# Optimization experiments

Hardware: AMD Instinct MI355X
Metric: run time of the kernel (lower is better)

The kernel has to match this reference:

```python
import jax, jax.numpy as jnp
import numpy as np

D_MODEL = 384
KSIZE = 3
B, L = 32, 512
LN_EPS = 1e-5


def _conv1d_same(x, w, b):
    # x: [B, C_in, L], w: [C_out, C_in, K] -> [B, C_out, L]
    y = jax.lax.conv_general_dilated(
        x, w, window_strides=(1,), padding='SAME',
        dimension_numbers=('NCH', 'OIH', 'NCH'))
    return y + b[None, :, None]


def _conv_fft_block(x, wa, ba, wb, bb):
    # Conv1D_FFT: transpose -> conv/relu -> conv/relu -> transpose back
    h = jnp.transpose(x, (0, 2, 1))            # [B, D, L]
    h = jax.nn.relu(_conv1d_same(h, wa, ba))
    h = jax.nn.relu(_conv1d_same(h, wb, bb))
    return jnp.transpose(h, (0, 2, 1))         # [B, L, D]


def _layernorm(x, g, b):
    mu = jnp.mean(x, axis=-1, keepdims=True)
    var = jnp.var(x, axis=-1, keepdims=True)
    return (x - mu) * jax.lax.rsqrt(var + LN_EPS) * g + b


def setup_inputs() -> dict:
    key = jax.random.key(0)
    ks = jax.random.split(key, 8)
    x = jax.random.normal(ks[0], (B, L, D_MODEL), dtype=jnp.float32)
    durations = jax.random.randint(ks[1], (B, L), 0, 8, dtype=jnp.int32)
    s = 0.02
    params = {
        'c1a_w': jax.random.normal(ks[2], (D_MODEL, D_MODEL, KSIZE), jnp.float32) * s,
        'c1a_b': jnp.zeros((D_MODEL,), jnp.float32),
        'c1b_w': jax.random.normal(ks[3], (D_MODEL, D_MODEL, KSIZE), jnp.float32) * s,
        'c1b_b': jnp.zeros((D_MODEL,), jnp.float32),
        'ln1_g': jnp.ones((D_MODEL,), jnp.float32),
        'ln1_b': jnp.zeros((D_MODEL,), jnp.float32),
        'c2a_w': jax.random.normal(ks[4], (D_MODEL, D_MODEL, KSIZE), jnp.float32) * s,
        'c2a_b': jnp.zeros((D_MODEL,), jnp.float32),
        'c2b_w': jax.random.normal(ks[5], (D_MODEL, D_MODEL, KSIZE), jnp.float32) * s,
        'c2b_b': jnp.zeros((D_MODEL,), jnp.float32),
        'ln2_g': jnp.ones((D_MODEL,), jnp.float32),
        'ln2_b': jnp.zeros((D_MODEL,), jnp.float32),
        'lin_w': jax.random.normal(ks[6], (D_MODEL, 1), jnp.float32) * s,
        'lin_b': jnp.zeros((1,), jnp.float32),
    }
    return {'x': x, 'durations': durations, **params}


def reference(x, durations, c1a_w, c1a_b, c1b_w, c1b_b, ln1_g, ln1_b,
              c2a_w, c2a_b, c2b_w, c2b_b, ln2_g, ln2_b, lin_w, lin_b):
    # --- DurationPredictor (dropout = identity, eval mode) ---
    h = _conv_fft_block(x, c1a_w, c1a_b, c1b_w, c1b_b)
    h = _layernorm(h, ln1_g, ln1_b)
    h = _conv_fft_block(h, c2a_w, c2a_b, c2b_w, c2b_b)
    h = _layernorm(h, ln2_g, ln2_b)
    dur_preds = (h @ lin_w + lin_b)[..., 0]      # [B, L]

    # --- LR: duration-based expansion via one-hot alignment matmul ---
    total = jnp.sum(durations, axis=-1)          # [B]
    T = int(jnp.max(total))                      # concrete (durations are input data)
    cum = jnp.cumsum(durations, axis=-1)         # [B, L]
    t = jnp.arange(T, dtype=cum.dtype)           # [T]
    # frame t belongs to phoneme j s.t. cum[j-1] <= t < cum[j]
    idx = jax.vmap(lambda c: jnp.searchsorted(c, t, side='right'))(cum)  # [B, T]
    mask = (t[None, :] < total[:, None]).astype(x.dtype)                 # [B, T]
    align = jax.nn.one_hot(idx, x.shape[1], dtype=x.dtype) * mask[:, :, None]  # [B, T, L]
    out = jnp.einsum('btl,bld->btd', align, x)   # [B, T, D]
    return (out, dur_preds)
```

## Files before the change

kernel.cpp:

```cpp
#include <hip/hip_runtime.h>

#define B_   32
#define L_   512
#define D_   384
#define M_   (B_*L_)
#define KTOT (D_*3)
#define LDW  392
#define BROWS 82
#define BUFE (BROWS*LDW)
#define RPBLK 1728
#define RPTOT (4*RPBLK)
#define SCAT  8192
#define ZT    (16*B_)

typedef __bf16 bf16x8 __attribute__((ext_vector_type(8)));
typedef float  floatx4 __attribute__((ext_vector_type(4)));

__global__ __launch_bounds__(256) void mega_prep_lr(const float* __restrict__ wa,
                                                    const float* __restrict__ wb,
                                                    const float* __restrict__ wc,
                                                    const float* __restrict__ wd,
                                                    __bf16* __restrict__ oa,
                                                    __bf16* __restrict__ ob,
                                                    __bf16* __restrict__ oc,
                                                    __bf16* __restrict__ od,
                                                    const int* __restrict__ dur,
                                                    const float* __restrict__ x,
                                                    float* __restrict__ out, int T)
{
    __shared__ int scum[512];
    int bx = blockIdx.x;

    if (bx < RPTOT) {
        int wi  = bx / RPBLK;
        int idx = (bx - wi * RPBLK) * 256 + threadIdx.x;
        const float* w; __bf16* o_;
        switch (wi) {
            case 0:  w = wa; o_ = oa; break;
            case 1:  w = wb; o_ = ob; break;
            case 2:  w = wc; o_ = oc; break;
            default: w = wd; o_ = od; break;
        }
        int j  = idx & 7;
        int l  = (idx >> 3) & 63;
        int ct = idx >> 9;
        int c  = ct / 24;
        int t  = ct - c * 24;
        int o  = t * 16 + (l & 15);
        int kflat = c * 32 + (l >> 4) * 8 + j;
        int s  = kflat / D_;
        int i  = kflat - s * D_;
        o_[idx] = (__bf16)w[(o * D_ + i) * 3 + s];
        return;
    }

    if (bx < RPTOT + SCAT) {
        int sx  = bx - RPTOT;
        int pl0 = sx * 2;
        int b   = pl0 >> 9;
        const int* db = dur + b * L_;
        if (threadIdx.x < 64) {
            int lane = threadIdx.x;
            int v[8], s = 0;
#pragma unroll
            for (int i = 0; i < 8; i++) { v[i] = db[lane * 8 + i]; s += v[i]; }
            int ex = s;
#pragma unroll
            for (int off = 1; off < 64; off <<= 1) {
                int n = __shfl_up(ex, off);
                if (lane >= off) ex += n;
            }
            ex -= s;
            int c = ex;
#pragma unroll
            for (int i = 0; i < 8; i++) { c += v[i]; scum[lane * 8 + i] = c; }
        }
        __syncthreads();
        int sub = threadIdx.x >> 7;
        int q   = threadIdx.x & 127;
        int l   = (pl0 & 511) + sub;
        int e = scum[l];
        int s = l ? scum[l - 1] : 0;
        if (e == s || q >= 96) return;
        int pl = b * L_ + l;
        float4 v = *(const float4*)(x + (size_t)pl * D_ + q * 4);
        float* ob_ = out + ((size_t)b * T) * D_ + q * 4;
        for (int t = s; t < e; ++t)
            *(float4*)(ob_ + (size_t)t * D_) = v;
        return;
    }

    int zb = bx - RPTOT - SCAT;
    int bxi = zb & 15;
    int b   = zb >> 4;
    if (threadIdx.x < 64) {
        int lane = threadIdx.x;
        int s = 0;
#pragma unroll
        for (int i = 0; i < 8; i++) s += dur[b * L_ + lane * 8 + i];
#pragma unroll
        for (int off = 1; off < 64; off <<= 1) s += __shfl_xor(s, off);
        if (lane == 0) scum[0] = s;
    }
    __syncthreads();
    int total = scum[0];
    int nfr = T - total;
    if (nfr <= 0) return;
    float* base = out + ((size_t)b * T + total) * D_;
    int n4 = nfr * 96;
    for (int i = bxi * 256 + threadIdx.x; i < n4; i += 4096) {
        int fr = i / 96, q = i - fr * 96;
        *(float4*)(base + (size_t)fr * D_ + q * 4) = make_float4(0.f, 0.f, 0.f, 0.f);
    }
}

__global__ __launch_bounds__(512, 1) void fused_predictor(
    const float* __restrict__ x,
    const __bf16* __restrict__ w1a, const float* __restrict__ b1a,
    const __bf16* __restrict__ w1b, const float* __restrict__ b1b,
    const float* __restrict__ g1,  const float* __restrict__ e1,
    const __bf16* __restrict__ w2a, const float* __restrict__ b2a,
    const __bf16* __restrict__ w2b, const float* __restrict__ b2b,
    const float* __restrict__ g2,  const float* __restrict__ e2,
    const float* __restrict__ lw,  const float* __restrict__ lb,
    float* __restrict__ out_dur)
{
    extern __shared__ char smem_raw[];
    __bf16* bufA = (__bf16*)smem_raw;
    __bf16* bufB = bufA + BUFE;
    float*  red1 = (float*)(bufB + BUFE);
    float*  red2 = red1 + BROWS * 8;
    float*  minv = red2 + BROWS * 8;

    const int m0 = blockIdx.x * 64;
    const int l0 = m0 & 511;
    const int b0 = m0 - l0;

    const int tid  = threadIdx.x;
    const int wave = tid >> 6;
    const int lane = tid & 63;
    const int quad = lane >> 4;
    const int lx   = lane & 15;
    const int ng   = wave & 3;
    const int mg   = wave >> 2;
    const int mtc  = mg ? 2 : 3;
    const int mtb  = mg ? 3 : 0;

    bf16x8 kz;
#pragma unroll
    for (int z = 0; z < 8; z++) kz[z] = (__bf16)0.f;

    for (int c = tid; c < BROWS * 48; c += 512) {
        int beta = c / 48, q = c - beta * 48;
        int l = l0 + beta - 9;
        bf16x8 v = kz;
        if ((unsigned)l < (unsigned)L_) {
            const float* xr = x + (size_t)(b0 + l) * D_ + q * 8;
            const float4 f0 = *(const float4*)xr;
            const float4 f1 = *(const float4*)(xr + 4);
            v[0] = (__bf16)f0.x; v[1] = (__bf16)f0.y; v[2] = (__bf16)f0.z; v[3] = (__bf16)f0.w;
            v[4] = (__bf16)f1.x; v[5] = (__bf16)f1.y; v[6] = (__bf16)f1.z; v[7] = (__bf16)f1.w;
        }
        *(bf16x8*)(&bufA[beta * LDW + q * 8]) = v;
    }
    for (int c = tid; c < 2 * 48; c += 512) {
        int beta = (c < 48) ? 0 : 81, q = c % 48;
        *(bf16x8*)(&bufB[beta * LDW + q * 8]) = kz;
    }
    __syncthreads();

    const int t0   = ng * 6;
    const int col0 = ng * 96 + lx;

    floatx4 acc[3][6];
    bf16x8  bg[3][6];

    for (int st = 0; st < 4; st++) {
        const __bf16* bin  = (st & 1) ? bufB : bufA;
        __bf16*       bout = (st & 1) ? bufA : bufB;
        const __bf16* Wp = (st == 0) ? w1a : (st == 1) ? w1b : (st == 2) ? w2a : w2b;
        const float*  bp = (st == 0) ? b1a : (st == 1) ? b1b : (st == 2) ? b2a : b2b;

#pragma unroll
        for (int mt = 0; mt < 3; mt++)
            if (mt < mtc)
#pragma unroll
                for (int ni = 0; ni < 6; ni++)
#pragma unroll
                    for (int r = 0; r < 4; r++) acc[mt][ni][r] = 0.f;

        const char* pb0 = (const char*)Wp + ((size_t)t0 * 64 + lane) * 16;
        auto loadB = [&](int buf, int n) {
            int it = n / 3, s = n - it * 3;
            const char* p = pb0 + (size_t)(s * 12 + it) * 24576;
#pragma unroll
            for (int ni = 0; ni < 6; ni++)
                bg[buf][ni] = *(const bf16x8*)(p + ni * 1024);
        };
        loadB(0, 0); loadB(1, 1);

        const __bf16* ab = bin + (mtb * 16 + lx) * LDW + quad * 8;
#pragma unroll
        for (int n = 0; n < 36; n++) {
            const int it = n / 3, s = n - it * 3;
            if (n + 2 < 36) loadB((n + 2) % 3, n + 2);
            bf16x8 af[3];
            af[0] = *(const bf16x8*)(ab + (s) * LDW + it * 32);
            af[1] = *(const bf16x8*)(ab + (16 + s) * LDW + it * 32);
            if (mtc == 3)
                af[2] = *(const bf16x8*)(ab + (32 + s) * LDW + it * 32);
            __builtin_amdgcn_s_setprio(1);
#pragma unroll
            for (int ni = 0; ni < 6; ni++) {
                acc[0][ni] = __builtin_amdgcn_mfma_f32_16x16x32_bf16(af[0], bg[n % 3][ni], acc[0][ni], 0, 0, 0);
                acc[1][ni] = __builtin_amdgcn_mfma_f32_16x16x32_bf16(af[1], bg[n % 3][ni], acc[1][ni], 0, 0, 0);
            }
            if (mtc == 3) {
#pragma unroll
                for (int ni = 0; ni < 6; ni++)
                    acc[2][ni] = __builtin_amdgcn_mfma_f32_16x16x32_bf16(af[2], bg[n % 3][ni], acc[2][ni], 0, 0, 0);
            }
            __builtin_amdgcn_s_setprio(0);
        }

        float bv[6];
#pragma unroll
        for (int ni = 0; ni < 6; ni++) bv[ni] = bp[col0 + ni * 16];
#pragma unroll
        for (int mt = 0; mt < 3; mt++)
            if (mt < mtc)
#pragma unroll
                for (int ni = 0; ni < 6; ni++)
#pragma unroll
                    for (int r = 0; r < 4; r++) {
                        float vv = acc[mt][ni][r] + bv[ni];
                        acc[mt][ni][r] = vv > 0.f ? vv : 0.f;
                    }

        if (st == 1 || st == 3) {
#pragma unroll
            for (int mt = 0; mt < 3; mt++)
                if (mt < mtc)
#pragma unroll
                    for (int r = 0; r < 4; r++) {
                        float s1 = 0.f, s2 = 0.f;
#pragma unroll
                        for (int ni = 0; ni < 6; ni++) {
                            s1 += acc[mt][ni][r];
                            s2 += acc[mt][ni][r] * acc[mt][ni][r];
                        }
#pragma unroll
                        for (int d = 1; d < 16; d <<= 1) {
                            s1 += __shfl_xor(s1, d);
                            s2 += __shfl_xor(s2, d);
                        }
                        if (lx == 0) {
                            int beta = (mtb + mt) * 16 + quad * 4 + r + 1;
                            red1[beta * 8 + wave] = s1;
                            red2[beta * 8 + wave] = s2;
                        }
                    }
            __syncthreads();
            if (tid < BROWS) {
                int tile = (tid - 1) >> 4;
                int base = (tile >= 3) ? 4 : 0;
                float s1 = 0.f, s2 = 0.f;
#pragma unroll
                for (int k = 0; k < 4; k++) { s1 += red1[tid * 8 + base + k]; s2 += red2[tid * 8 + base + k]; }
                float mean = s1 * (1.f / D_);
                float var  = s2 * (1.f / D_) - mean * mean;
                minv[tid * 2]     = mean;
                minv[tid * 2 + 1] = rsqrtf(var + 1e-5f);
            }
            __syncthreads();
            const float* gp = (st == 1) ? g1 : g2;
            const float* ep = (st == 1) ? e1 : e2;
            float gv[6], ev[6];
#pragma unroll
            for (int ni = 0; ni < 6; ni++) { gv[ni] = gp[col0 + ni * 16]; ev[ni] = ep[col0 + ni * 16]; }
#pragma unroll
            for (int mt = 0; mt < 3; mt++)
                if (mt < mtc)
#pragma unroll
                    for (int r = 0; r < 4; r++) {
                        int beta = (mtb + mt) * 16 + quad * 4 + r + 1;
                        float mean = minv[beta * 2], inv = minv[beta * 2 + 1];
#pragma unroll
                        for (int ni = 0; ni < 6; ni++)
                            acc[mt][ni][r] = (acc[mt][ni][r] - mean) * inv * gv[ni] + ev[ni];
                    }
            if (st == 1) {
#pragma unroll
                for (int mt = 0; mt < 3; mt++)
                    if (mt < mtc)
#pragma unroll
                        for (int r = 0; r < 4; r++) {
                            int beta = (mtb + mt) * 16 + quad * 4 + r + 1;
                            bool ok = (unsigned)(l0 + beta - 9) < (unsigned)L_;
#pragma unroll
                            for (int ni = 0; ni < 6; ni++)
                                bout[beta * LDW + col0 + ni * 16] = (__bf16)(ok ? acc[mt][ni][r] : 0.f);
                        }
            } else {
                float lwv[6];
#pragma unroll
                for (int ni = 0; ni < 6; ni++) lwv[ni] = lw[col0 + ni * 16];
#pragma unroll
                for (int mt = 0; mt < 3; mt++)
                    if (mt < mtc)
#pragma unroll
                        for (int r = 0; r < 4; r++) {
                            float p = 0.f;
#pragma unroll
                            for (int ni = 0; ni < 6; ni++) p += acc[mt][ni][r] * lwv[ni];
#pragma unroll
                            for (int d = 1; d < 16; d <<= 1) p += __shfl_xor(p, d);
                            if (lx == 0) {
                                int beta = (mtb + mt) * 16 + quad * 4 + r + 1;
                                red1[beta * 8 + wave] = p;
                            }
                        }
                __syncthreads();
                if (tid < 64) {
                    int beta = tid + 9;
                    int tile = (beta - 1) >> 4;
                    int base = (tile >= 3) ? 4 : 0;
                    float sacc = lb[0];
#pragma unroll
                    for (int k = 0; k < 4; k++) sacc += red1[beta * 8 + base + k];
                    out_dur[m0 + tid] = sacc;
                }
            }
        } else {
#pragma unroll
            for (int mt = 0; mt < 3; mt++)
                if (mt < mtc)
#pragma unroll
                    for (int r = 0; r < 4; r++) {
                        int beta = (mtb + mt) * 16 + quad * 4 + r + 1;
                        bool ok = (unsigned)(l0 + beta - 9) < (unsigned)L_;
#pragma unroll
                        for (int ni = 0; ni < 6; ni++)
                            bout[beta * LDW + col0 + ni * 16] = (__bf16)(ok ? acc[mt][ni][r] : 0.f);
                    }
        }
        __syncthreads();
    }
}

extern "C" void kernel_launch(void* const* d_in, const int* in_sizes, int n_in,
                              void* d_out, int out_size, void* d_ws, size_t ws_size,
                              hipStream_t stream) {
    const float* x       = (const float*)d_in[0];
    const int*   dur     = (const int*)d_in[1];
    const float* c1a_w   = (const float*)d_in[2];
    const float* c1a_b   = (const float*)d_in[3];
    const float* c1b_w   = (const float*)d_in[4];
    const float* c1b_b   = (const float*)d_in[5];
    const float* ln1_g   = (const float*)d_in[6];
    const float* ln1_b   = (const float*)d_in[7];
    const float* c2a_w   = (const float*)d_in[8];
    const float* c2a_b   = (const float*)d_in[9];
    const float* c2b_w   = (const float*)d_in[10];
    const float* c2b_b   = (const float*)d_in[11];
    const float* ln2_g   = (const float*)d_in[12];
    const float* ln2_b   = (const float*)d_in[13];
    const float* lin_w   = (const float*)d_in[14];
    const float* lin_b   = (const float*)d_in[15];

    const int T = (out_size - B_ * L_) / (B_ * D_);
    float* out_gather = (float*)d_out;
    float* out_dur    = (float*)d_out + (size_t)B_ * T * D_;

    char* p = (char*)d_ws;
    __bf16* w1a = (__bf16*)p; p += (size_t)D_ * KTOT * 2;
    __bf16* w1b = (__bf16*)p; p += (size_t)D_ * KTOT * 2;
    __bf16* w2a = (__bf16*)p; p += (size_t)D_ * KTOT * 2;
    __bf16* w2b = (__bf16*)p; p += (size_t)D_ * KTOT * 2;

    mega_prep_lr<<<RPTOT + SCAT + ZT, 256, 0, stream>>>(
        c1a_w, c1b_w, c2a_w, c2b_w, w1a, w1b, w2a, w2b,
        dur, x, out_gather, T);

    const size_t smem = (size_t)2 * BUFE * 2 + (BROWS * 8 * 2 + BROWS * 2) * 4;
    static bool attr_set = false;
    if (!attr_set) {
        hipFuncSetAttribute((const void*)fused_predictor,
                            hipFuncAttributeMaxDynamicSharedMemorySize, (int)smem);
        attr_set = true;
    }
    fused_predictor<<<256, 512, smem, stream>>>(
        x, w1a, c1a_b, w1b, c1b_b, ln1_g, ln1_b,
        w2a, c2a_b, w2b, c2b_b, ln2_g, ln2_b,
        lin_w, lin_b, out_dur);
}
```

Before: 228.3 us.

## Merge LR expansion into predictor kernel and single-buffer activations for 2 blocks/CU

Moves the duration-based scatter and zero-fill work out of the weight-repack kernel and into extra blocks of the fused predictor launch, so the memory-bound LR expansion can run alongside the compute-bound conv stack. The ping-pong activation buffers are collapsed into one shared buffer, with an extra barrier before write-back, roughly halving LDS use so launch bounds allow two blocks per CU. This trades extra synchronization per stage and possible register pressure under the tighter occupancy bound for overlap and better latency hiding.

```diff
diff --git a/kernel.cpp b/kernel.cpp
--- a/kernel.cpp
+++ b/kernel.cpp
@@ -10,111 +10,46 @@
 #define BUFE (BROWS*LDW)
 #define RPBLK 1728
 #define RPTOT (4*RPBLK)
-#define SCAT  8192
-#define ZT    (16*B_)
+#define FUSE  256
+#define SCB   4096
+#define ZTB   (8*B_)
+#define SMEM_MEGA (BUFE*2 + (BROWS*8*2 + BROWS*2)*4)
 
 typedef __bf16 bf16x8 __attribute__((ext_vector_type(8)));
 typedef float  floatx4 __attribute__((ext_vector_type(4)));
 
-__global__ __launch_bounds__(256) void mega_prep_lr(const float* __restrict__ wa,
-                                                    const float* __restrict__ wb,
-                                                    const float* __restrict__ wc,
-                                                    const float* __restrict__ wd,
-                                                    __bf16* __restrict__ oa,
-                                                    __bf16* __restrict__ ob,
-                                                    __bf16* __restrict__ oc,
-                                                    __bf16* __restrict__ od,
-                                                    const int* __restrict__ dur,
-                                                    const float* __restrict__ x,
-                                                    float* __restrict__ out, int T)
+__global__ __launch_bounds__(256) void repack_kernel(const float* __restrict__ wa,
+                                                     const float* __restrict__ wb,
+                                                     const float* __restrict__ wc,
+                                                     const float* __restrict__ wd,
+                                                     __bf16* __restrict__ oa,
+                                                     __bf16* __restrict__ ob,
+                                                     __bf16* __restrict__ oc,
+                                                     __bf16* __restrict__ od)
 {
-    __shared__ int scum[512];
     int bx = blockIdx.x;
-
-    if (bx < RPTOT) {
-        int wi  = bx / RPBLK;
-        int idx = (bx - wi * RPBLK) * 256 + threadIdx.x;
-        const float* w; __bf16* o_;
-        switch (wi) {
-            case 0:  w = wa; o_ = oa; break;
-            case 1:  w = wb; o_ = ob; break;
-            case 2:  w = wc; o_ = oc; break;
-            default: w = wd; o_ = od; break;
-        }
-        int j  = idx & 7;
-        int l  = (idx >> 3) & 63;
-        int ct = idx >> 9;
-        int c  = ct / 24;
-        int t  = ct - c * 24;
-        int o  = t * 16 + (l & 15);
-        int kflat = c * 32 + (l >> 4) * 8 + j;
-        int s  = kflat / D_;
-        int i  = kflat - s * D_;
-        o_[idx] = (__bf16)w[(o * D_ + i) * 3 + s];
-        return;
-    }
-
-    if (bx < RPTOT + SCAT) {
-        int sx  = bx - RPTOT;
-        int pl0 = sx * 2;
-        int b   = pl0 >> 9;
-        const int* db = dur + b * L_;
-        if (threadIdx.x < 64) {
-            int lane = threadIdx.x;
-            int v[8], s = 0;
-#pragma unroll
-            for (int i = 0; i < 8; i++) { v[i] = db[lane * 8 + i]; s += v[i]; }
-            int ex = s;
-#pragma unroll
-            for (int off = 1; off < 64; off <<= 1) {
-                int n = __shfl_up(ex, off);
-                if (lane >= off) ex += n;
-            }
-            ex -= s;
-            int c = ex;
-#pragma unroll
-            for (int i = 0; i < 8; i++) { c += v[i]; scum[lane * 8 + i] = c; }
-        }
-        __syncthreads();
-        int sub = threadIdx.x >> 7;
-        int q   = threadIdx.x & 127;
-        int l   = (pl0 & 511) + sub;
-        int e = scum[l];
-        int s = l ? scum[l - 1] : 0;
-        if (e == s || q >= 96) return;
-        int pl = b * L_ + l;
-        float4 v = *(const float4*)(x + (size_t)pl * D_ + q * 4);
-        float* ob_ = out + ((size_t)b * T) * D_ + q * 4;
-        for (int t = s; t < e; ++t)
-            *(float4*)(ob_ + (size_t)t * D_) = v;
-        return;
-    }
-
-    int zb = bx - RPTOT - SCAT;
-    int bxi = zb & 15;
-    int b   = zb >> 4;
-    if (threadIdx.x < 64) {
-        int lane = threadIdx.x;
-        int s = 0;
-#pragma unroll
-        for (int i = 0; i < 8; i++) s += dur[b * L_ + lane * 8 + i];
-#pragma unroll
-        for (int off = 1; off < 64; off <<= 1) s += __shfl_xor(s, off);
-        if (lane == 0) scum[0] = s;
-    }
-    __syncthreads();
-    int total = scum[0];
-    int nfr = T - total;
-    if (nfr <= 0) return;
-    float* base = out + ((size_t)b * T + total) * D_;
-    int n4 = nfr * 96;
-    for (int i = bxi * 256 + threadIdx.x; i < n4; i += 4096) {
-        int fr = i / 96, q = i - fr * 96;
-        *(float4*)(base + (size_t)fr * D_ + q * 4) = make_float4(0.f, 0.f, 0.f, 0.f);
-    }
+    int wi  = bx / RPBLK;
+    int idx = (bx - wi * RPBLK) * 256 + threadIdx.x;
+    const float* w; __bf16* o_;
+    switch (wi) {
+        case 0:  w = wa; o_ = oa; break;
+        case 1:  w = wb; o_ = ob; break;
+        case 2:  w = wc; o_ = oc; break;
+        default: w = wd; o_ = od; break;
+    }
+    int j  = idx & 7;
+    int l  = (idx >> 3) & 63;
+    int ct = idx >> 9;
+    int c  = ct / 24;
+    int t  = ct - c * 24;
+    int o  = t * 16 + (l & 15);
+    int kflat = c * 32 + (l >> 4) * 8 + j;
+    int s  = kflat / D_;
+    int i  = kflat - s * D_;
+    o_[idx] = (__bf16)w[(o * D_ + i) * 3 + s];
 }
 
-__global__ __launch_bounds__(512, 1) void fused_predictor(
+__global__ __launch_bounds__(512, 2) void mega_kernel(
     const float* __restrict__ x,
     const __bf16* __restrict__ w1a, const float* __restrict__ b1a,
     const __bf16* __restrict__ w1b, const float* __restrict__ b1b,
@@ -123,12 +58,75 @@
     const __bf16* __restrict__ w2b, const float* __restrict__ b2b,
     const float* __restrict__ g2,  const float* __restrict__ e2,
     const float* __restrict__ lw,  const float* __restrict__ lb,
-    float* __restrict__ out_dur)
+    float* __restrict__ out_dur,
+    const int* __restrict__ dur,
+    float* __restrict__ out_lr, int T)
 {
     extern __shared__ char smem_raw[];
-    __bf16* bufA = (__bf16*)smem_raw;
-    __bf16* bufB = bufA + BUFE;
-    float*  red1 = (float*)(bufB + BUFE);
+
+    if (blockIdx.x >= FUSE) {
+        int* scum = (int*)smem_raw;
+        if (blockIdx.x < FUSE + SCB) {
+            int sx = blockIdx.x - FUSE;
+            int b  = sx >> 7;
+            const int* db = dur + b * L_;
+            if (threadIdx.x < 64) {
+                int lane = threadIdx.x;
+                int v[8], s = 0;
+#pragma unroll
+                for (int i = 0; i < 8; i++) { v[i] = db[lane * 8 + i]; s += v[i]; }
+                int ex = s;
+#pragma unroll
+                for (int off = 1; off < 64; off <<= 1) {
+                    int n = __shfl_up(ex, off);
+                    if (lane >= off) ex += n;
+                }
+                ex -= s;
+                int c = ex;
+#pragma unroll
+                for (int i = 0; i < 8; i++) { c += v[i]; scum[lane * 8 + i] = c; }
+            }
+            __syncthreads();
+            int sub = threadIdx.x >> 7;
+            int q   = threadIdx.x & 127;
+            int l   = (sx & 127) * 4 + sub;
+            int e = scum[l];
+            int s = l ? scum[l - 1] : 0;
+            if (e == s || q >= 96) return;
+            int pl = b * L_ + l;
+            float4 v = *(const float4*)(x + (size_t)pl * D_ + q * 4);
+            float* ob_ = out_lr + ((size_t)b * T) * D_ + q * 4;
+            for (int t = s; t < e; ++t)
+                *(float4*)(ob_ + (size_t)t * D_) = v;
+            return;
+        }
+        int zb  = blockIdx.x - FUSE - SCB;
+        int bxi = zb & 7;
+        int b   = zb >> 3;
+        if (threadIdx.x < 64) {
+            int lane = threadIdx.x;
+            int s = 0;
+#pragma unroll
+            for (int i = 0; i < 8; i++) s += dur[b * L_ + lane * 8 + i];
+#pragma unroll
+            for (int off = 1; off < 64; off <<= 1) s += __shfl_xor(s, off);
+            if (lane == 0) scum[0] = s;
+        }
+        __syncthreads();
+        int total = scum[0];
+        int nfr = T - total;
+        if (nfr <= 0) return;
+        float* base = out_lr + ((size_t)b * T + total) * D_;
+        int n4 = nfr * 96;
+        for (int i = bxi * 512 + threadIdx.x; i < n4; i += 4096) {
+            int fr = i / 96, q = i - fr * 96;
+            *(float4*)(base + (size_t)fr * D_ + q * 4) = make_float4(0.f, 0.f, 0.f, 0.f);
+        }
+        return;
+    }
+
+    __bf16* buf  = (__bf16*)smem_raw;
+    float*  red1 = (float*)(buf + BUFE);
     float*  red2 = red1 + BROWS * 8;
     float*  minv = red2 + BROWS * 8;
 
@@ -161,11 +159,7 @@
             v[0] = (__bf16)f0.x; v[1] = (__bf16)f0.y; v[2] = (__bf16)f0.z; v[3] = (__bf16)f0.w;
             v[4] = (__bf16)f1.x; v[5] = (__bf16)f1.y; v[6] = (__bf16)f1.z; v[7] = (__bf16)f1.w;
         }
-        *(bf16x8*)(&bufA[beta * LDW + q * 8]) = v;
-    }
-    for (int c = tid; c < 2 * 48; c += 512) {
-        int beta = (c < 48) ? 0 : 81, q = c % 48;
-        *(bf16x8*)(&bufB[beta * LDW + q * 8]) = kz;
+        *(bf16x8*)(&buf[beta * LDW + q * 8]) = v;
     }
     __syncthreads();
 
@@ -176,8 +170,6 @@
     bf16x8  bg[3][6];
 
     for (int st = 0; st < 4; st++) {
-        const __bf16* bin  = (st & 1) ? bufB : bufA;
-        __bf16*       bout = (st & 1) ? bufA : bufB;
         const __bf16* Wp = (st == 0) ? w1a : (st == 1) ? w1b : (st == 2) ? w2a : w2b;
         const float*  bp = (st == 0) ? b1a : (st == 1) ? b1b : (st == 2) ? b2a : b2b;
 
@@ -190,16 +182,16 @@
                     for (int r = 0; r < 4; r++) acc[mt][ni][r] = 0.f;
 
         const char* pb0 = (const char*)Wp + ((size_t)t0 * 64 + lane) * 16;
-        auto loadB = [&](int buf, int n) {
+        auto loadB = [&](int bi, int n) {
             int it = n / 3, s = n - it * 3;
             const char* p = pb0 + (size_t)(s * 12 + it) * 24576;
 #pragma unroll
             for (int ni = 0; ni < 6; ni++)
-                bg[buf][ni] = *(const bf16x8*)(p + ni * 1024);
+                bg[bi][ni] = *(const bf16x8*)(p + ni * 1024);
         };
         loadB(0, 0); loadB(1, 1);
 
-        const __bf16* ab = bin + (mtb * 16 + lx) * LDW + quad * 8;
+        const __bf16* ab = buf + (mtb * 16 + lx) * LDW + quad * 8;
 #pragma unroll
         for (int n = 0; n < 36; n++) {
             const int it = n / 3, s = n - it * 3;
@@ -299,7 +291,7 @@
                             bool ok = (unsigned)(l0 + beta - 9) < (unsigned)L_;
 #pragma unroll
                             for (int ni = 0; ni < 6; ni++)
-                                bout[beta * LDW + col0 + ni * 16] = (__bf16)(ok ? acc[mt][ni][r] : 0.f);
+                                buf[beta * LDW + col0 + ni * 16] = (__bf16)(ok ? acc[mt][ni][r] : 0.f);
                         }
             } else {
                 float lwv[6];
@@ -332,6 +324,7 @@
                 }
             }
         } else {
+            __syncthreads();
 #pragma unroll
             for (int mt = 0; mt < 3; mt++)
                 if (mt < mtc)
@@ -341,7 +334,7 @@
                         bool ok = (unsigned)(l0 + beta - 9) < (unsigned)L_;
 #pragma unroll
                         for (int ni = 0; ni < 6; ni++)
-                            bout[beta * LDW + col0 + ni * 16] = (__bf16)(ok ? acc[mt][ni][r] : 0.f);
+                            buf[beta * LDW + col0 + ni * 16] = (__bf16)(ok ? acc[mt][ni][r] : 0.f);
                     }
         }
         __syncthreads();
@@ -378,19 +371,17 @@
     __bf16* w2a = (__bf16*)p; p += (size_t)D_ * KTOT * 2;
     __bf16* w2b = (__bf16*)p; p += (size_t)D_ * KTOT * 2;
 
-    mega_prep_lr<<<RPTOT + SCAT + ZT, 256, 0, stream>>>(
-        c1a_w, c1b_w, c2a_w, c2b_w, w1a, w1b, w2a, w2b,
-        dur, x, out_gather, T);
-
-    const size_t smem = (size_t)2 * BUFE * 2 + (BROWS * 8 * 2 + BROWS * 2) * 4;
+    repack_kernel<<<RPTOT, 256, 0, stream>>>(
+        c1a_w, c1b_w, c2a_w, c2b_w, w1a, w1b, w2a, w2b);
+
     static bool attr_set = false;
     if (!attr_set) {
-        hipFuncSetAttribute((const void*)fused_predictor,
-                            hipFuncAttributeMaxDynamicSharedMemorySize, (int)smem);
+        hipFuncSetAttribute((const void*)mega_kernel,
+                            hipFuncAttributeMaxDynamicSharedMemorySize, (int)SMEM_MEGA);
         attr_set = true;
     }
-    fused_predictor<<<256, 512, smem, stream>>>(
+    mega_kernel<<<FUSE + SCB + ZTB, 512, SMEM_MEGA, stream>>>(
         x, w1a, c1a_b, w1b, c1b_b, ln1_g, ln1_b,
         w2a, c2a_b, w2b, c2b_b, ln2_g, ln2_b,
-        lin_w, lin_b, out_dur);
+        lin_w, lin_b, out_dur, dur, out_gather, T);
 }
```

Result: slower. 242.0 us (+6.0%).
